# Optimization experiments

Hardware: AMD Instinct MI355X
Metric: run time of the kernel (lower is better)

Reference implementation:

```python
import jax, jax.numpy as jnp
import numpy as np

NUM_HEADS = 16
NUM_GROUPS = 4
HEAD_DIM = 128  # d_out // num_heads


def setup_inputs() -> dict:
    key = jax.random.key(0)
    ks = jax.random.split(key, 6)
    b, t, d_in, d_out = 4, 2048, 2048, 2048
    kv_dim = NUM_GROUPS * HEAD_DIM
    s = 0.02
    return {
        "x": jax.random.normal(ks[0], (b, t, d_in), jnp.float32),
        "Wq": jax.random.normal(ks[1], (d_in, d_out), jnp.float32) * s,
        "Wk": jax.random.normal(ks[2], (d_in, kv_dim), jnp.float32) * s,
        "Wv": jax.random.normal(ks[3], (d_in, kv_dim), jnp.float32) * s,
        "Wo": jax.random.normal(ks[4], (d_out, d_out), jnp.float32) * s,
        "bo": jnp.zeros((d_out,), jnp.float32),
    }


def reference(x, Wq, Wk, Wv, Wo, bo):
    b, t, _ = x.shape
    H, G, D = NUM_HEADS, NUM_GROUPS, HEAD_DIM
    P = H // G  # heads_per_group
    # Projections
    q = (x @ Wq).reshape(b, t, G, P, D)          # head h = g*P + p matches repeat_interleave
    k = (x @ Wk).reshape(b, t, G, D)
    v = (x @ Wv).reshape(b, t, G, D)
    # Scores: [b, G, P, tq, tk] (grouped form of repeat_interleave over heads)
    scores = jnp.einsum('bqgpd,bkgd->bgpqk', q, k)
    # Causal mask: q_pos < k_pos -> -inf
    qpos = jnp.arange(t)
    mask = qpos[:, None] < qpos[None, :]  # [tq, tk], True above diagonal
    scores = jnp.where(mask[None, None, None], -jnp.inf, scores)
    attn = jax.nn.softmax(scores / np.float32(np.sqrt(D)), axis=-1)
    ctx = jnp.einsum('bgpqk,bkgd->bqgpd', attn, v)  # [b, t, G, P, D]
    ctx = ctx.reshape(b, t, H * D)
    return ctx @ Wo + bo
```

## Files before the change

kernel.cpp:

```cpp
#include <hip/hip_runtime.h>
#include <hip/hip_bf16.h>
#include <stdint.h>
#include <math.h>

#define T_SEQ 2048
#define D_MODEL 2048
#define KV_DIM 512
#define QKV_LD 3072
#define NHEADS 16
#define HDIM 128
#define BATCH 4
#define MT (BATCH * T_SEQ)

typedef __attribute__((ext_vector_type(4))) float f32x4;
typedef __attribute__((ext_vector_type(8))) __bf16 bf16x8;
typedef __attribute__((ext_vector_type(4))) __bf16 bf16x4;
typedef __attribute__((ext_vector_type(8))) unsigned short u16x8;
typedef __attribute__((ext_vector_type(4))) unsigned short u16x4;
typedef __attribute__((ext_vector_type(4))) short s16x4;

static __device__ __forceinline__ unsigned short f32_bf16(float f) {
  unsigned u = __float_as_uint(f);
  u += 0x7fff + ((u >> 16) & 1);
  return (unsigned short)(u >> 16);
}

static __device__ __forceinline__ void gload_lds16(const void* g, void* l) {
  __builtin_amdgcn_global_load_lds(
      (__attribute__((address_space(1))) void*)(const_cast<void*>(g)),
      (__attribute__((address_space(3))) void*)l, 16, 0, 0);
}

static __device__ __forceinline__ f32x4 mfma16(bf16x8 a, bf16x8 b, f32x4 c) {
  return __builtin_amdgcn_mfma_f32_16x16x32_bf16(a, b, c, 0, 0, 0);
}

static __device__ __forceinline__ f32x4 mfma16x16(u16x4 a, u16x4 b, f32x4 c) {
#if __has_builtin(__builtin_amdgcn_mfma_f32_16x16x16bf16_1k)
  return __builtin_amdgcn_mfma_f32_16x16x16bf16_1k(
      __builtin_bit_cast(s16x4, a), __builtin_bit_cast(s16x4, b), c, 0, 0, 0);
#elif __has_builtin(__builtin_amdgcn_mfma_f32_16x16x16_bf16)
  return __builtin_amdgcn_mfma_f32_16x16x16_bf16(
      __builtin_bit_cast(bf16x4, a), __builtin_bit_cast(bf16x4, b), c, 0, 0, 0);
#else
  f32x4 d;
  asm("v_mfma_f32_16x16x16_bf16 %0, %1, %2, %3" : "=v"(d) : "v"(a), "v"(b), "v"(c));
  return d;
#endif
}

#define VIDX(d, c) (((((d) << 3) + ((c) ^ ((d) & 7))) << 3))

__global__ void cvt_kernel(const float* __restrict__ in, unsigned short* __restrict__ out, int n4) {
  int i = blockIdx.x * 256 + threadIdx.x;
  if (i >= n4) return;
  f32x4 v = ((const f32x4*)in)[i];
  u16x4 o;
#pragma unroll
  for (int j = 0; j < 4; ++j) o[j] = f32_bf16(v[j]);
  ((u16x4*)out)[i] = o;
}

__global__ void transpose_kernel(const float* __restrict__ W, unsigned short* __restrict__ Wt,
                                 int K, int N) {
  __shared__ float tile[32][33];
  int bx = blockIdx.x * 32;
  int by = blockIdx.y * 32;
  int tx = threadIdx.x, ty = threadIdx.y;
#pragma unroll
  for (int i = 0; i < 32; i += 8)
    tile[ty + i][tx] = W[(size_t)(by + ty + i) * N + bx + tx];
  __syncthreads();
#pragma unroll
  for (int i = 0; i < 32; i += 8)
    Wt[(size_t)(bx + ty + i) * K + by + tx] = f32_bf16(tile[tx][ty + i]);
}

template <typename OutT, bool HAS_BIAS>
__global__ __launch_bounds__(256, 2) void gemm_bt_kernel(
    const unsigned short* __restrict__ A, const unsigned short* __restrict__ Bt,
    OutT* __restrict__ C, const float* __restrict__ bias, int M, int N, int K) {
  __shared__ unsigned short As[128 * 32];
  __shared__ unsigned short Bs[128 * 32];
  const int tid = threadIdx.x;
  const int wave = tid >> 6, lane = tid & 63;
  const int lr = lane & 15, lh = lane >> 4;
  const int wr = (wave >> 1) * 64, wc = (wave & 1) * 64;
  const size_t ar0 = (size_t)blockIdx.y * 128;
  const size_t br0 = (size_t)blockIdx.x * 128;

  f32x4 acc[4][4] = {};

  for (int k0 = 0; k0 < K; k0 += 32) {
#pragma unroll
    for (int is = 0; is < 2; ++is) {
      const int c = is * 4 + wave;
      const int u = c * 64 + lane;
      const int r = u >> 2;
      const int kk = (u & 3) * 8;
      gload_lds16(A + (ar0 + r) * K + (k0 + kk), (char*)As + c * 1024);
      gload_lds16(Bt + (br0 + r) * K + (k0 + kk), (char*)Bs + c * 1024);
    }
    __syncthreads();
    bf16x8 af[4], bf[4];
#pragma unroll
    for (int m = 0; m < 4; ++m)
      af[m] = *(const bf16x8*)&As[(wr + m * 16 + lr) * 32 + lh * 8];
#pragma unroll
    for (int n = 0; n < 4; ++n)
      bf[n] = *(const bf16x8*)&Bs[(wc + n * 16 + lr) * 32 + lh * 8];
#pragma unroll
    for (int m = 0; m < 4; ++m)
#pragma unroll
      for (int n = 0; n < 4; ++n)
        acc[m][n] = mfma16(af[m], bf[n], acc[m][n]);
    __syncthreads();
  }

#pragma unroll
  for (int m = 0; m < 4; ++m) {
#pragma unroll
    for (int n = 0; n < 4; ++n) {
      const size_t col = br0 + wc + n * 16 + lr;
      float bv = 0.0f;
      if constexpr (HAS_BIAS) bv = bias[col];
#pragma unroll
      for (int r = 0; r < 4; ++r) {
        const size_t row = ar0 + wr + m * 16 + lh * 4 + r;
        const float val = acc[m][n][r] + bv;
        if constexpr (sizeof(OutT) == 2)
          ((unsigned short*)C)[row * N + col] = f32_bf16(val);
        else
          ((float*)C)[row * N + col] = val;
      }
    }
  }
}

static __device__ __forceinline__ void softmax_step(
    const f32x4 st[4], u16x4 pr[4], float& m_run, float& l_run,
    f32x4* oaccq, bool maskT, int kv0, int qglob, int lh) {
  float p[4][4];
#pragma unroll
  for (int n = 0; n < 4; ++n)
#pragma unroll
    for (int r = 0; r < 4; ++r) {
      float val = st[n][r];
      if (maskT && (kv0 + n * 16 + lh * 4 + r > qglob)) val = -1e30f;
      p[n][r] = val;
    }
  float pm[4];
#pragma unroll
  for (int n = 0; n < 4; ++n)
    pm[n] = fmaxf(fmaxf(p[n][0], p[n][1]), fmaxf(p[n][2], p[n][3]));
  float pmax = fmaxf(fmaxf(pm[0], pm[1]), fmaxf(pm[2], pm[3]));
  pmax = fmaxf(pmax, __shfl_xor(pmax, 16));
  pmax = fmaxf(pmax, __shfl_xor(pmax, 32));
  const bool resc = __any(pmax > m_run + 8.0f);
  float alpha = 1.0f;
  if (resc) {
    const float mnew = fmaxf(m_run, pmax);
    alpha = exp2f(m_run - mnew);
    m_run = mnew;
  }
  float rsum = 0.0f;
#pragma unroll
  for (int n = 0; n < 4; ++n) {
#pragma unroll
    for (int r = 0; r < 4; ++r) {
      p[n][r] = exp2f(p[n][r] - m_run);
      rsum += p[n][r];
    }
    __hip_bfloat162 t0 = __float22bfloat162_rn(make_float2(p[n][0], p[n][1]));
    __hip_bfloat162 t1 = __float22bfloat162_rn(make_float2(p[n][2], p[n][3]));
    unsigned lo, hi;
    __builtin_memcpy(&lo, &t0, 4);
    __builtin_memcpy(&hi, &t1, 4);
    unsigned long long both = (unsigned long long)lo | ((unsigned long long)hi << 32);
    u16x4 pk;
    __builtin_memcpy(&pk, &both, 8);
    pr[n] = pk;
  }
  rsum += __shfl_xor(rsum, 16);
  rsum += __shfl_xor(rsum, 32);
  if (resc) {
    l_run = l_run * alpha + rsum;
#pragma unroll
    for (int r = 0; r < 4; ++r) {
      const float a = __shfl(alpha, lh * 4 + r);
#pragma unroll
      for (int nd = 0; nd < 8; ++nd) oaccq[nd][r] *= a;
    }
  } else {
    l_run += rsum;
  }
}

__global__ __launch_bounds__(256, 2) void attn_kernel(
    const unsigned short* __restrict__ qkv, unsigned short* __restrict__ ctx) {
  const int lin = blockIdx.x;
  const int xcd = lin & 7;
  const int j = lin >> 3;
  const int sel = j & 1;
  const int i = j >> 1;
  const int p = i & 3;
  const int qt = 15 - (i >> 2);
  const int s = xcd * 2 + sel;
  const int b = s >> 2, g = s & 3;
  const int h = g * 4 + p;
  const int tid = threadIdx.x;
  const int wave = tid >> 6, lane = tid & 63;
  const int lr = lane & 15, lh = lane >> 4;
  const int qb = qt * 128;
  const int qrow0 = qb + wave * 16;
  const int qrow1 = qb + 64 + wave * 16;

  __shared__ unsigned short Ks[64 * 128];
  __shared__ unsigned short Vts[128 * 64];

  const int vr0 = (tid & 31) * 2;
  const int vc0 = (tid >> 5) * 16;
  const int vcu = vr0 >> 3, vcw = vr0 & 7;

  const unsigned short* qrow_base = qkv + (size_t)b * T_SEQ * QKV_LD;
  const unsigned short* kbase = qrow_base + D_MODEL + g * HDIM;
  const unsigned short* vbase = qrow_base + D_MODEL + KV_DIM + g * HDIM;

  const float QS = 0.1275174f;
  bf16x8 aq[2][4];
  {
    const unsigned short* qp0 = qrow_base + (size_t)(qrow0 + lr) * QKV_LD + h * HDIM + lh * 8;
    const unsigned short* qp1 = qrow_base + (size_t)(qrow1 + lr) * QKV_LD + h * HDIM + lh * 8;
#pragma unroll
    for (int kk = 0; kk < 4; ++kk) {
      u16x8 r0 = *(const u16x8*)(qp0 + kk * 32);
      u16x8 r1 = *(const u16x8*)(qp1 + kk * 32);
      u16x8 o0, o1;
#pragma unroll
      for (int jj = 0; jj < 8; ++jj) {
        o0[jj] = f32_bf16(__uint_as_float((unsigned)r0[jj] << 16) * QS);
        o1[jj] = f32_bf16(__uint_as_float((unsigned)r1[jj] << 16) * QS);
      }
      aq[0][kk] = __builtin_bit_cast(bf16x8, o0);
      aq[1][kk] = __builtin_bit_cast(bf16x8, o1);
    }
  }

  f32x4 oacc[2][8] = {};
  float m_run0 = -1e30f, l_run0 = 0.0f, m_run1 = -1e30f, l_run1 = 0.0f;

  const int nt = 2 * qt + 2;

  for (int t = 0; t < nt; ++t) {
    const int kv0 = t * 64;
    __syncthreads();
#pragma unroll
    for (int is = 0; is < 4; ++is) {
      const int c = is * 4 + wave;
      const int u = c * 64 + lane;
      const int vu = u ^ ((u >> 4) & 7);
      const int r = vu >> 4;
      const int cc = (vu & 15) * 8;
      gload_lds16(kbase + (size_t)(kv0 + r) * QKV_LD + cc, (char*)Ks + c * 1024);
    }
    {
      const unsigned short* vp = vbase + (size_t)(kv0 + vr0) * QKV_LD + vc0;
      u16x8 va0 = *(const u16x8*)(vp);
      u16x8 va1 = *(const u16x8*)(vp + 8);
      u16x8 vb0 = *(const u16x8*)(vp + QKV_LD);
      u16x8 vb1 = *(const u16x8*)(vp + QKV_LD + 8);
#pragma unroll
      for (int jj = 0; jj < 8; ++jj) {
        const int d0 = vc0 + jj, d1 = vc0 + 8 + jj;
        *(unsigned int*)&Vts[VIDX(d0, vcu) + vcw] =
            (unsigned int)va0[jj] | ((unsigned int)vb0[jj] << 16);
        *(unsigned int*)&Vts[VIDX(d1, vcu) + vcw] =
            (unsigned int)va1[jj] | ((unsigned int)vb1[jj] << 16);
      }
    }
    __syncthreads();

    const bool live0 = (t < nt - 1);
    const bool mask0 = (t == nt - 2);
    const bool mask1 = (t == nt - 1);

    f32x4 st0[4] = {}, st1[4] = {};
    __builtin_amdgcn_s_setprio(1);
#pragma unroll
    for (int n = 0; n < 4; ++n) {
      const int rr = n * 16 + lr;
#pragma unroll
      for (int kk = 0; kk < 4; ++kk) {
        const int lu = rr * 16 + kk * 4 + lh;
        const int pu = lu ^ (rr & 7);
        const bf16x8 ak = *(const bf16x8*)((const char*)Ks + pu * 16);
        if (live0) st0[n] = mfma16(ak, aq[0][kk], st0[n]);
        st1[n] = mfma16(ak, aq[1][kk], st1[n]);
      }
    }
    __builtin_amdgcn_s_setprio(0);

    u16x4 pr0[4], pr1[4];
    if (live0)
      softmax_step(st0, pr0, m_run0, l_run0, oacc[0], mask0, kv0, qrow0 + lr, lh);
    softmax_step(st1, pr1, m_run1, l_run1, oacc[1], mask1, kv0, qrow1 + lr, lh);

    __builtin_amdgcn_s_setprio(1);
#pragma unroll
    for (int n = 0; n < 4; ++n) {
      const int cb = n * 2 + (lh >> 1);
      const int off = (lh & 1) * 4;
#pragma unroll
      for (int nd = 0; nd < 8; ++nd) {
        const int d = nd * 16 + lr;
        const u16x4 vf = *(const u16x4*)&Vts[VIDX(d, cb) + off];
        if (live0) oacc[0][nd] = mfma16x16(pr0[n], vf, oacc[0][nd]);
        oacc[1][nd] = mfma16x16(pr1[n], vf, oacc[1][nd]);
      }
    }
    __builtin_amdgcn_s_setprio(0);
  }

#pragma unroll
  for (int m = 0; m < 2; ++m) {
    const float lm = (m == 0) ? l_run0 : l_run1;
    const int qrow = (m == 0) ? qrow0 : qrow1;
    unsigned short* cp = ctx + ((size_t)b * T_SEQ + qrow) * D_MODEL + h * HDIM;
#pragma unroll
    for (int r = 0; r < 4; ++r) {
      const float inv = 1.0f / __shfl(lm, lh * 4 + r);
#pragma unroll
      for (int nd = 0; nd < 8; ++nd)
        cp[(size_t)(lh * 4 + r) * D_MODEL + nd * 16 + lr] =
            f32_bf16(oacc[m][nd][r] * inv);
    }
  }
}

extern "C" void kernel_launch(void* const* d_in, const int* in_sizes, int n_in,
                              void* d_out, int out_size, void* d_ws, size_t ws_size,
                              hipStream_t stream) {
  const float* x = (const float*)d_in[0];
  const float* Wq = (const float*)d_in[1];
  const float* Wk = (const float*)d_in[2];
  const float* Wv = (const float*)d_in[3];
  const float* Wo = (const float*)d_in[4];
  const float* bo = (const float*)d_in[5];
  float* out = (float*)d_out;

  char* ws = (char*)d_ws;
  unsigned short* xb = (unsigned short*)(ws + 0);
  unsigned short* ctx = (unsigned short*)(ws + 0);
  unsigned short* qkv = (unsigned short*)(ws + 33554432);
  unsigned short* WqkvT = (unsigned short*)(ws + 83886080);
  unsigned short* WoT = (unsigned short*)(ws + 96468992);

  const int n4 = MT * D_MODEL / 4;
  cvt_kernel<<<(n4 + 255) / 256, 256, 0, stream>>>(x, xb, n4);
  dim3 tb(32, 8);
  transpose_kernel<<<dim3(D_MODEL / 32, D_MODEL / 32), tb, 0, stream>>>(
      Wq, WqkvT, D_MODEL, D_MODEL);
  transpose_kernel<<<dim3(KV_DIM / 32, D_MODEL / 32), tb, 0, stream>>>(
      Wk, WqkvT + (size_t)D_MODEL * D_MODEL, D_MODEL, KV_DIM);
  transpose_kernel<<<dim3(KV_DIM / 32, D_MODEL / 32), tb, 0, stream>>>(
      Wv, WqkvT + (size_t)(D_MODEL + KV_DIM) * D_MODEL, D_MODEL, KV_DIM);
  transpose_kernel<<<dim3(D_MODEL / 32, D_MODEL / 32), tb, 0, stream>>>(
      Wo, WoT, D_MODEL, D_MODEL);

  gemm_bt_kernel<unsigned short, false><<<dim3(QKV_LD / 128, MT / 128), 256, 0, stream>>>(
      xb, WqkvT, qkv, nullptr, MT, QKV_LD, D_MODEL);

  attn_kernel<<<1024, 256, 0, stream>>>(qkv, ctx);

  gemm_bt_kernel<float, true><<<dim3(D_MODEL / 128, MT / 128), 256, 0, stream>>>(
      ctx, WoT, out, bo, MT, D_MODEL, D_MODEL);
}
```

Measured before the change: 407.1 us.

## Replace GEMM with 256x256 double-buffered, swizzled, pipelined 8-wave kernel

```diff
diff --git a/kernel.cpp b/kernel.cpp
--- a/kernel.cpp
+++ b/kernel.cpp
@@ -49,6 +49,12 @@
 #endif
 }
 
+static __device__ __forceinline__ void barx() {
+  asm volatile("" ::: "memory");
+  __builtin_amdgcn_s_barrier();
+  asm volatile("" ::: "memory");
+}
+
 #define VIDX(d, c) (((((d) << 3) + ((c) ^ ((d) & 7))) << 3))
 
 __global__ void cvt_kernel(const float* __restrict__ in, unsigned short* __restrict__ out, int n4) {
@@ -77,57 +83,116 @@
 }
 
 template <typename OutT, bool HAS_BIAS>
-__global__ __launch_bounds__(256, 2) void gemm_bt_kernel(
+__global__ __launch_bounds__(512, 2) void gemm256_kernel(
     const unsigned short* __restrict__ A, const unsigned short* __restrict__ Bt,
     OutT* __restrict__ C, const float* __restrict__ bias, int M, int N, int K) {
-  __shared__ unsigned short As[128 * 32];
-  __shared__ unsigned short Bs[128 * 32];
+  __shared__ unsigned short As[2][16384];
+  __shared__ unsigned short Bs[2][16384];
   const int tid = threadIdx.x;
   const int wave = tid >> 6, lane = tid & 63;
   const int lr = lane & 15, lh = lane >> 4;
-  const int wr = (wave >> 1) * 64, wc = (wave & 1) * 64;
-  const size_t ar0 = (size_t)blockIdx.y * 128;
-  const size_t br0 = (size_t)blockIdx.x * 128;
-
-  f32x4 acc[4][4] = {};
-
-  for (int k0 = 0; k0 < K; k0 += 32) {
-#pragma unroll
-    for (int is = 0; is < 2; ++is) {
-      const int c = is * 4 + wave;
-      const int u = c * 64 + lane;
-      const int r = u >> 2;
-      const int kk = (u & 3) * 8;
-      gload_lds16(A + (ar0 + r) * K + (k0 + kk), (char*)As + c * 1024);
-      gload_lds16(Bt + (br0 + r) * K + (k0 + kk), (char*)Bs + c * 1024);
-    }
-    __syncthreads();
-    bf16x8 af[4], bf[4];
-#pragma unroll
-    for (int m = 0; m < 4; ++m)
-      af[m] = *(const bf16x8*)&As[(wr + m * 16 + lr) * 32 + lh * 8];
-#pragma unroll
-    for (int n = 0; n < 4; ++n)
-      bf[n] = *(const bf16x8*)&Bs[(wc + n * 16 + lr) * 32 + lh * 8];
-#pragma unroll
-    for (int m = 0; m < 4; ++m)
-#pragma unroll
-      for (int n = 0; n < 4; ++n)
-        acc[m][n] = mfma16(af[m], bf[n], acc[m][n]);
-    __syncthreads();
-  }
-
-#pragma unroll
-  for (int m = 0; m < 4; ++m) {
+  const int wm = wave >> 2, wn = wave & 3;
+
+  const int gx = gridDim.x;
+  const int nwg = gx * gridDim.y;
+  int flat = blockIdx.y * gx + blockIdx.x;
+  flat = (flat & 7) * (nwg >> 3) + (flat >> 3);
+  const int bx = flat % gx, by = flat / gx;
+
+  const unsigned short* Ag = A + (size_t)by * 256 * K;
+  const unsigned short* Bg = Bt + (size_t)bx * 256 * K;
+
+  const int srow_lo = lane >> 2;
+  const int sbcol = ((lane & 3) * 16) ^ ((srow_lo & 8) << 2);
+  const int scol = sbcol >> 1;
+
+#define STAGE_HALF(SRC, DST, HK)                                            \
+  {                                                                         \
+    _Pragma("unroll") for (int s = 0; s < 2; ++s) {                         \
+      const int jj = s * 8 + wave;                                          \
+      gload_lds16((SRC) + (size_t)(jj * 16 + srow_lo) * K + (HK) * 32 + scol, \
+                  (char*)(DST) + (jj * 2 + (HK)) * 1024);                   \
+    }                                                                       \
+  }
+
+  const int aoff = lr * 32 + ((lh * 8) ^ ((lr & 8) << 1));
+  const int abase = wm * 8 * 1024;
+  const int bbase = wn * 4 * 1024;
+
+  f32x4 acc[8][4] = {};
+  bf16x8 af[4], bf[4];
+
+#define PH_READ_A(MH, KS)                                                   \
+  {                                                                         \
+    _Pragma("unroll") for (int m = 0; m < 4; ++m)                           \
+      af[m] = *(const bf16x8*)&As[cur][abase + ((MH)*4 + m) * 1024 + (KS)*512 + aoff]; \
+  }
+#define PH_READ_B(KS)                                                       \
+  {                                                                         \
+    _Pragma("unroll") for (int n = 0; n < 4; ++n)                           \
+      bf[n] = *(const bf16x8*)&Bs[cur][bbase + n * 1024 + (KS)*512 + aoff]; \
+  }
+#define PH_MFMA(MH)                                                         \
+  {                                                                         \
+    __builtin_amdgcn_s_setprio(1);                                          \
+    _Pragma("unroll") for (int m = 0; m < 4; ++m)                           \
+      _Pragma("unroll") for (int n = 0; n < 4; ++n)                         \
+        acc[(MH)*4 + m][n] = mfma16(af[m], bf[n], acc[(MH)*4 + m][n]);      \
+    __builtin_amdgcn_s_setprio(0);                                          \
+  }
+
+  STAGE_HALF(Ag, As[0], 0);
+  STAGE_HALF(Bg, Bs[0], 0);
+  STAGE_HALF(Ag, As[0], 1);
+  STAGE_HALF(Bg, Bs[0], 1);
+  asm volatile("s_waitcnt vmcnt(4)" ::: "memory");
+  barx();
+
+  const int NT = K >> 6;
+  for (int t = 0; t < NT; ++t) {
+    const int cur = t & 1;
+    const bool pf = (t + 1 < NT);
+    const unsigned short* An = Ag + (size_t)(t + 1) * 64;
+    const unsigned short* Bn = Bg + (size_t)(t + 1) * 64;
+    unsigned short* Ad = As[cur ^ 1];
+    unsigned short* Bd = Bs[cur ^ 1];
+
+    PH_READ_A(0, 0); PH_READ_B(0);
+    if (pf) STAGE_HALF(An, Ad, 0);
+    barx(); PH_MFMA(0); barx();
+
+    PH_READ_A(1, 0);
+    if (pf) {
+      STAGE_HALF(Bn, Bd, 0);
+      asm volatile("s_waitcnt vmcnt(4)" ::: "memory");
+    } else {
+      asm volatile("s_waitcnt vmcnt(0)" ::: "memory");
+    }
+    barx(); PH_MFMA(1); barx();
+
+    PH_READ_A(0, 1); PH_READ_B(1);
+    if (pf) STAGE_HALF(An, Ad, 1);
+    barx(); PH_MFMA(0); barx();
+
+    PH_READ_A(1, 1);
+    if (pf) {
+      STAGE_HALF(Bn, Bd, 1);
+      asm volatile("s_waitcnt vmcnt(4)" ::: "memory");
+    }
+    barx(); PH_MFMA(1); barx();
+  }
+
+#pragma unroll
+  for (int m8 = 0; m8 < 8; ++m8) {
 #pragma unroll
     for (int n = 0; n < 4; ++n) {
-      const size_t col = br0 + wc + n * 16 + lr;
+      const size_t col = (size_t)bx * 256 + wn * 64 + n * 16 + lr;
       float bv = 0.0f;
       if constexpr (HAS_BIAS) bv = bias[col];
 #pragma unroll
       for (int r = 0; r < 4; ++r) {
-        const size_t row = ar0 + wr + m * 16 + lh * 4 + r;
-        const float val = acc[m][n][r] + bv;
+        const size_t row = (size_t)by * 256 + wm * 128 + m8 * 16 + lh * 4 + r;
+        const float val = acc[m8][n][r] + bv;
         if constexpr (sizeof(OutT) == 2)
           ((unsigned short*)C)[row * N + col] = f32_bf16(val);
         else
@@ -135,6 +200,10 @@
       }
     }
   }
+#undef STAGE_HALF
+#undef PH_READ_A
+#undef PH_READ_B
+#undef PH_MFMA
 }
 
 static __device__ __forceinline__ void softmax_step(
@@ -367,11 +436,11 @@
   transpose_kernel<<<dim3(D_MODEL / 32, D_MODEL / 32), tb, 0, stream>>>(
       Wo, WoT, D_MODEL, D_MODEL);
 
-  gemm_bt_kernel<unsigned short, false><<<dim3(QKV_LD / 128, MT / 128), 256, 0, stream>>>(
+  gemm256_kernel<unsigned short, false><<<dim3(QKV_LD / 256, MT / 256), 512, 0, stream>>>(
       xb, WqkvT, qkv, nullptr, MT, QKV_LD, D_MODEL);
 
   attn_kernel<<<1024, 256, 0, stream>>>(qkv, ctx);
 
-  gemm_bt_kernel<float, true><<<dim3(D_MODEL / 128, MT / 128), 256, 0, stream>>>(
+  gemm256_kernel<float, true><<<dim3(D_MODEL / 256, MT / 256), 512, 0, stream>>>(
       ctx, WoT, out, bo, MT, D_MODEL, D_MODEL);
 }
```

After: 399.5 us. About the same (-1.9%).
